# Kernel tuning notes

Hardware: AMD Instinct MI355X
Metric: run time of the kernel (lower is better)

The kernel has to match this reference:

```python
import jax, jax.numpy as jnp
import numpy as np

HIDDEN = 4096
NH = 32          # num query heads
NKV = 8          # num kv heads
HD = HIDDEN // NH  # 128
THETA = 10000.0
L = 4096         # llama_context_len (attention-sink window)
BS = 16          # paged KV block size
B = 16           # decode batch
MAXB = 385       # blocks per sequence
NBLOCKS = B * MAXB
CTX = 6145       # context_len for every sequence (num_past = 6144)


def rope(x, pos):
    """Neox-style RoPE. x: [..., H, HD]; pos: broadcastable to x.shape[:-2]."""
    half = HD // 2
    inv_freq = 1.0 / (THETA ** (jnp.arange(half, dtype=jnp.float32) * 2.0 / HD))
    ang = pos.astype(jnp.float32)[..., None] * inv_freq      # [..., half]
    cos = jnp.cos(ang)[..., None, :]                          # [..., 1, half]
    sin = jnp.sin(ang)[..., None, :]
    x1, x2 = x[..., :half], x[..., half:]
    return jnp.concatenate([x1 * cos - x2 * sin, x2 * cos + x1 * sin], axis=-1)


def setup_inputs() -> dict:
    key = jax.random.key(0)
    ks = jax.random.split(key, 6)
    hidden_states = jax.random.normal(ks[0], (B, HIDDEN), jnp.float32)
    positions = jax.random.randint(ks[1], (B,), 0, CTX).astype(jnp.int32)
    key_cache = jax.random.normal(ks[2], (NBLOCKS, NKV, HD, BS), jnp.float32)
    value_cache = jax.random.normal(ks[3], (NBLOCKS, NKV, HD, BS), jnp.float32)
    block_tables = jnp.arange(B * MAXB, dtype=jnp.int32).reshape(B, MAXB)
    w_qkv = jax.random.normal(ks[4], (HIDDEN, (NH + 2 * NKV) * HD), jnp.float32) * 0.02
    w_o = jax.random.normal(ks[5], (NH * HD, HIDDEN), jnp.float32) * 0.02
    return {
        "positions": positions,
        "hidden_states": hidden_states,
        "key_cache": key_cache,
        "value_cache": value_cache,
        "block_tables": block_tables,
        "context_len": CTX,
        "w_qkv": w_qkv,
        "w_o": w_o,
    }


def reference(positions, hidden_states, key_cache, value_cache, block_tables,
              context_len, w_qkv, w_o):
    # ---- qkv projection + split ----
    qkv = hidden_states @ w_qkv
    q, k, v = jnp.split(qkv, [NH * HD, NH * HD + NKV * HD], axis=-1)
    # ---- clamp positions to sink window and rope current q, k ----
    clamped = jnp.minimum(positions, L - 1)
    q = rope(q.reshape(B, NH, HD), clamped)          # [B, NH, HD]
    k = rope(k.reshape(B, NKV, HD), clamped)         # [B, NKV, HD]
    v = v.reshape(B, NKV, HD)

    # ---- static sink-window geometry (context_len is a Python int) ----
    num_past = context_len - 1
    blocks_to_ignore = (num_past - L) // BS + 1
    start = num_past - L + 1 + BS
    end = num_past

    # capped block table: token t<BS -> sink block bt[0];
    # t>=BS -> bt[blocks_to_ignore + t//BS]
    t = jnp.arange(L)
    logical = jnp.where(t < BS, 0, blocks_to_ignore + t // BS)   # [L]
    offset = t % BS                                              # [L]
    abs_pos = logical * BS + offset                              # [L] absolute position in seq

    phys = block_tables[:, logical]                              # [B, L]
    K = key_cache[phys, :, :, offset]                            # [B, L, NKV, HD]
    V = value_cache[phys, :, :, offset]

    # ---- sink RoPE rewrite: keys in [start, end) get an extra rotation at abs_pos-start ----
    rot_mask = (abs_pos >= start) & (abs_pos < end)
    K = jnp.where(rot_mask[None, :, None, None], rope(K, abs_pos - start), K)

    # ---- current token's freshly-rotated k/v occupy slot abs_pos == num_past ----
    cur = (abs_pos == num_past)
    K = jnp.where(cur[None, :, None, None], k[:, None, :, :], K)
    V = jnp.where(cur[None, :, None, None], v[:, None, :, :], V)

    # ---- GQA paged-decode attention over the 4096-token capped window ----
    valid = abs_pos <= num_past                                  # [L]
    G = NH // NKV
    qg = q.reshape(B, NKV, G, HD)
    scores = jnp.einsum('bkgd,blkd->bkgl', qg, K) * (HD ** -0.5)
    scores = jnp.where(valid[None, None, None, :], scores, jnp.finfo(scores.dtype).min)
    p = jax.nn.softmax(scores, axis=-1)
    attn = jnp.einsum('bkgl,blkd->bkgd', p, V).reshape(B, NH * HD)
    return attn @ w_o


if __name__ == "__main__":
    out = reference(**setup_inputs())
    print(out.shape, out.dtype)
```

## Files before the change

### kernel.cpp

```cpp
#include <hip/hip_runtime.h>
#include <math.h>

#define B_      16
#define NH      32
#define NKV     8
#define HD      128
#define GQ      4
#define LWIN    4096
#define BS      16
#define MAXB    385
#define HIDDEN  4096
#define QKV_COLS 6144
#define TAB_N   4100
#define T_CUR   4080
#define KS      64
#define NSPLIT  64
#define NCHUNK  8
#define SCALE   0.088388347648318447f
#define LOG1E4  9.210340371976184
#define TWO_PI  6.283185307179586
#define INV_2PI 0.15915494309189535

typedef float f4v __attribute__((ext_vector_type(4)));

__global__ __launch_bounds__(128, 1) void k_gemm_qkv(
    const float* __restrict__ X, const float* __restrict__ W,
    float* __restrict__ part,
    float* __restrict__ ctab, float* __restrict__ stab,
    float* __restrict__ pk, float* __restrict__ pv) {
  int tid = threadIdx.x;
  int k0 = blockIdx.y * KS;
  int n4 = (blockIdx.x * 128 + tid) * 4;
  f4v acc[B_];
#pragma unroll
  for (int b = 0; b < B_; b++) acc[b] = (f4v){0.f, 0.f, 0.f, 0.f};
  const float* wp = W + (size_t)k0 * QKV_COLS + n4;
  const float* xp = X + k0;
#pragma unroll
  for (int batch = 0; batch < KS / 16; batch++) {
    f4v w[16];
#pragma unroll
    for (int i = 0; i < 16; i++)
      w[i] = *(const f4v*)&wp[(size_t)(batch * 16 + i) * QKV_COLS];
#pragma unroll
    for (int i = 0; i < 16; i++) {
      int kk = batch * 16 + i;
#pragma unroll
      for (int b = 0; b < B_; b++) {
        float x = xp[b * HIDDEN + kk];
        acc[b][0] = fmaf(x, w[i][0], acc[b][0]);
        acc[b][1] = fmaf(x, w[i][1], acc[b][1]);
        acc[b][2] = fmaf(x, w[i][2], acc[b][2]);
        acc[b][3] = fmaf(x, w[i][3], acc[b][3]);
      }
    }
  }
  float* pp = part + (size_t)blockIdx.y * B_ * QKV_COLS + n4;
#pragma unroll
  for (int b = 0; b < B_; b++) *(f4v*)&pp[(size_t)b * QKV_COLS] = acc[b];

  int idx = (blockIdx.y * gridDim.x + blockIdx.x) * 128 + tid;
  if (idx < 64 * (TAB_N / 4)) {
    int d = idx / (TAB_N / 4);
    int q = idx - d * (TAB_N / 4);
    int i0 = q * 4;
    double f = exp(-(double)d / 64.0 * LOG1E4);
    double a = (double)(i0 - 1) * f;
    double rev = a * INV_2PI;
    rev -= rint(rev);
    float r = (float)(rev * TWO_PI);
    float c = cosf(r), s = sinf(r);
    float ff = (float)f;
    float cf = cosf(ff), sf = sinf(ff);
    int base = d * TAB_N + i0;
    ctab[base] = c; stab[base] = s;
#pragma unroll
    for (int j = 1; j < 4; j++) {
      float cn = c * cf - s * sf;
      float sn = s * cf + c * sf;
      c = cn; s = sn;
      ctab[base + j] = c; stab[base + j] = s;
    }
  }
  for (int z = idx; z < B_ * NKV * HD * BS; z += 98304) { pk[z] = 0.f; pv[z] = 0.f; }
}

__global__ __launch_bounds__(256) void k_qkv_finish(
    const float* __restrict__ part, const int* __restrict__ positions,
    const float* __restrict__ ctab, const float* __restrict__ stab,
    float* __restrict__ qout, float* __restrict__ pk, float* __restrict__ pv) {
  int idx = blockIdx.x * 256 + threadIdx.x;
  int b = idx / 3584;
  int u = idx - b * 3584;
  if (b >= B_) return;
  if (u < 2560) {
    int h = u >> 6, j = u & 63;
    int c1 = h * 128 + j;
    int c2 = c1 + 64;
    float s1 = 0.f, s2 = 0.f;
#pragma unroll 8
    for (int ky = 0; ky < NSPLIT; ky++) {
      const float* p = part + ((size_t)ky * B_ + b) * QKV_COLS;
      s1 += p[c1];
      s2 += p[c2];
    }
    int pos = min(positions[b], LWIN - 1);
    float c = ctab[j * TAB_N + pos + 1];
    float s = stab[j * TAB_N + pos + 1];
    float o1 = s1 * c - s2 * s;
    float o2 = s2 * c + s1 * s;
    if (h < NH) {
      qout[b * HIDDEN + c1] = o1;
      qout[b * HIDDEN + c2] = o2;
    } else {
      int kv = h - NH;
      pk[((b * NKV + kv) * HD + j) * BS] = o1;
      pk[((b * NKV + kv) * HD + j + 64) * BS] = o2;
    }
  } else {
    int vi = u - 2560;
    int kv = vi >> 7, d = vi & 127;
    int col = 5120 + vi;
    float s = 0.f;
#pragma unroll 8
    for (int ky = 0; ky < NSPLIT; ky++)
      s += part[((size_t)ky * B_ + b) * QKV_COLS + col];
    pv[((b * NKV + kv) * HD + d) * BS] = s;
  }
}

__global__ __launch_bounds__(128, 1) void k_attn(
    const float* __restrict__ kc, const float* __restrict__ vc,
    const int* __restrict__ bt, const float* __restrict__ qbuf,
    const float* __restrict__ pk, const float* __restrict__ pv,
    const float* __restrict__ ctab, const float* __restrict__ stab,
    float* __restrict__ partial) {
  __shared__ __align__(16) float qT[HD][GQ];
  __shared__ __align__(16) float p_s[512][GQ];
  __shared__ float redm[2][GQ];
  __shared__ float redl[2][GQ];
  __shared__ const float* kbase[32];
  __shared__ const float* vbase[32];

  int bx = blockIdx.x;
  int b = bx & 15, kv = bx >> 4;
  int chunk = blockIdx.y;
  int tid = threadIdx.x;
  int lane = tid & 63, wave = tid >> 6;

  for (int i = tid; i < GQ * HD; i += 128) {
    int g = i >> 7, d = i & 127;
    qT[d][g] = qbuf[b * HIDDEN + (kv * GQ + g) * HD + d];
  }
  if (tid < 32) {
    int tb = chunk * 32 + tid;
    if (tb == 255) {
      kbase[tid] = pk + (size_t)(b * NKV + kv) * (HD * BS);
      vbase[tid] = pv + (size_t)(b * NKV + kv) * (HD * BS);
    } else {
      int lg = (tb == 0) ? 0 : (129 + tb);
      size_t off = ((size_t)bt[b * MAXB + lg] * NKV + kv) * (HD * BS);
      kbase[tid] = kc + off;
      vbase[tid] = vc + off;
    }
  }
  __syncthreads();

  int blk_i = lane & 15, qq = lane >> 4;
  int t0 = chunk * 512 + wave * 256 + blk_i * 16 + qq * 4;
  const float* kb = kbase[wave * 16 + blk_i] + qq * 4;
  bool rot = (t0 >= 16) && (t0 < T_CUR);
  const float* ctp = ctab + t0;
  const float* stp = stab + t0;

  float sc[GQ][4];
#pragma unroll
  for (int g = 0; g < GQ; g++)
#pragma unroll
    for (int c = 0; c < 4; c++) sc[g][c] = 0.f;

#pragma unroll
  for (int batch = 0; batch < 8; batch++) {
    f4v k1[8], k2[8], cv[8], sv[8];
#pragma unroll
    for (int i = 0; i < 8; i++) {
      int d = batch * 8 + i;
      k1[i] = *(const f4v*)(kb + d * BS);
      k2[i] = *(const f4v*)(kb + (d + 64) * BS);
      cv[i] = *(const f4v*)(ctp + d * TAB_N);
      sv[i] = *(const f4v*)(stp + d * TAB_N);
    }
#pragma unroll
    for (int i = 0; i < 8; i++) {
      int d = batch * 8 + i;
      float4 q1 = *(const float4*)&qT[d][0];
      float4 q2 = *(const float4*)&qT[d + 64][0];
      float qg1[4] = {q1.x, q1.y, q1.z, q1.w};
      float qg2[4] = {q2.x, q2.y, q2.z, q2.w};
#pragma unroll
      for (int c = 0; c < 4; c++) {
        float cc = rot ? cv[i][c] : 1.f;
        float ss = rot ? sv[i][c] : 0.f;
        float r1 = k1[i][c] * cc - k2[i][c] * ss;
        float r2 = k2[i][c] * cc + k1[i][c] * ss;
#pragma unroll
        for (int g = 0; g < GQ; g++)
          sc[g][c] = fmaf(qg1[g], r1, fmaf(qg2[g], r2, sc[g][c]));
      }
    }
  }

  float mloc[GQ];
#pragma unroll
  for (int g = 0; g < GQ; g++) {
    float m = -3e38f;
#pragma unroll
    for (int c = 0; c < 4; c++) {
      float s = (t0 + c <= T_CUR) ? sc[g][c] * SCALE : -3e38f;
      sc[g][c] = s;
      m = fmaxf(m, s);
    }
#pragma unroll
    for (int off = 1; off < 64; off <<= 1) m = fmaxf(m, __shfl_xor(m, off, 64));
    mloc[g] = m;
  }
  if (lane == 0) {
#pragma unroll
    for (int g = 0; g < GQ; g++) redm[wave][g] = mloc[g];
  }
  __syncthreads();
  float mb[GQ];
#pragma unroll
  for (int g = 0; g < GQ; g++) mb[g] = fmaxf(redm[0][g], redm[1][g]);

  float4 prc[4];
  float ls[GQ] = {0.f, 0.f, 0.f, 0.f};
#pragma unroll
  for (int c = 0; c < 4; c++) {
    float p0 = __expf(sc[0][c] - mb[0]);
    float p1 = __expf(sc[1][c] - mb[1]);
    float p2 = __expf(sc[2][c] - mb[2]);
    float p3 = __expf(sc[3][c] - mb[3]);
    ls[0] += p0; ls[1] += p1; ls[2] += p2; ls[3] += p3;
    prc[c] = make_float4(p0, p1, p2, p3);
  }
#pragma unroll
  for (int g = 0; g < GQ; g++) {
    float v = ls[g];
#pragma unroll
    for (int off = 1; off < 64; off <<= 1) v += __shfl_xor(v, off, 64);
    ls[g] = v;
  }
  if (lane == 0) {
#pragma unroll
    for (int g = 0; g < GQ; g++) redl[wave][g] = ls[g];
  }
  int trow = t0 - chunk * 512;
#pragma unroll
  for (int c = 0; c < 4; c++) *(float4*)&p_s[trow + c][0] = prc[c];
  __syncthreads();

  float acc0 = 0.f, acc1 = 0.f, acc2 = 0.f, acc3 = 0.f;
  int d_own = tid;
#pragma unroll
  for (int bt4 = 0; bt4 < 8; bt4++) {
    f4v vr[4][4];
#pragma unroll
    for (int t = 0; t < 4; t++) {
      const float* vb = vbase[bt4 * 4 + t] + d_own * BS;
      vr[t][0] = *(const f4v*)(vb);
      vr[t][1] = *(const f4v*)(vb + 4);
      vr[t][2] = *(const f4v*)(vb + 8);
      vr[t][3] = *(const f4v*)(vb + 12);
    }
#pragma unroll
    for (int t = 0; t < 4; t++) {
      const float* pp = &p_s[(bt4 * 4 + t) * 16][0];
#pragma unroll
      for (int jq = 0; jq < 4; jq++) {
#pragma unroll
        for (int j = 0; j < 4; j++) {
          float4 pj = *(const float4*)(pp + (jq * 4 + j) * GQ);
          float vv = vr[t][jq][j];
          acc0 = fmaf(pj.x, vv, acc0);
          acc1 = fmaf(pj.y, vv, acc1);
          acc2 = fmaf(pj.z, vv, acc2);
          acc3 = fmaf(pj.w, vv, acc3);
        }
      }
    }
  }

  int pid = b * NKV + kv;
  float* pw = partial + ((size_t)pid * NCHUNK + chunk) * (GQ * 130);
  pw[0 * 130 + 2 + d_own] = acc0;
  pw[1 * 130 + 2 + d_own] = acc1;
  pw[2 * 130 + 2 + d_own] = acc2;
  pw[3 * 130 + 2 + d_own] = acc3;
  if (tid == 0) {
#pragma unroll
    for (int g = 0; g < GQ; g++) {
      pw[g * 130 + 0] = mb[g];
      pw[g * 130 + 1] = redl[0][g] + redl[1][g];
    }
  }
}

__global__ __launch_bounds__(128, 1) void k_gemm_o(
    const float* __restrict__ apart, const float* __restrict__ W,
    float* __restrict__ part) {
  __shared__ __align__(16) float xs[B_][KS];
  __shared__ float wexp[B_][NCHUNK];
  __shared__ float lw[B_];

  int tid = threadIdx.x;
  int k0 = blockIdx.y * KS;
  int h = k0 >> 7, kv = h >> 2, g = h & 3, d0 = k0 & 127;

  if (tid < B_) {
    int b = tid;
    const float* pb = apart + ((size_t)(b * NKV + kv) * NCHUNK) * (GQ * 130) + g * 130;
    float M = -3e38f;
#pragma unroll
    for (int c = 0; c < NCHUNK; c++) M = fmaxf(M, pb[c * (GQ * 130)]);
    float L = 0.f;
#pragma unroll
    for (int c = 0; c < NCHUNK; c++) {
      float w = __expf(pb[c * (GQ * 130)] - M);
      wexp[b][c] = w;
      L = fmaf(pb[c * (GQ * 130) + 1], w, L);
    }
    lw[b] = L;
  }
  __syncthreads();

#pragma unroll
  for (int it = 0; it < 8; it++) {
    int item = it * 128 + tid;
    int b = item >> 6, kk = item & 63;
    const float* pb = apart + ((size_t)(b * NKV + kv) * NCHUNK) * (GQ * 130) + g * 130 + 2 + d0 + kk;
    float val = 0.f;
#pragma unroll
    for (int c = 0; c < NCHUNK; c++) val = fmaf(pb[c * (GQ * 130)], wexp[b][c], val);
    xs[b][kk] = val / lw[b];
  }
  __syncthreads();

  int n4 = (blockIdx.x * 128 + tid) * 4;
  f4v acc[B_];
#pragma unroll
  for (int b = 0; b < B_; b++) acc[b] = (f4v){0.f, 0.f, 0.f, 0.f};
  const float* wp = W + (size_t)k0 * HIDDEN + n4;
#pragma unroll
  for (int batch = 0; batch < KS / 16; batch++) {
    f4v w[16];
#pragma unroll
    for (int i = 0; i < 16; i++)
      w[i] = *(const f4v*)&wp[(size_t)(batch * 16 + i) * HIDDEN];
#pragma unroll
    for (int i = 0; i < 16; i++) {
      int kk = batch * 16 + i;
#pragma unroll
      for (int b = 0; b < B_; b++) {
        float x = xs[b][kk];
        acc[b][0] = fmaf(x, w[i][0], acc[b][0]);
        acc[b][1] = fmaf(x, w[i][1], acc[b][1]);
        acc[b][2] = fmaf(x, w[i][2], acc[b][2]);
        acc[b][3] = fmaf(x, w[i][3], acc[b][3]);
      }
    }
  }
  float* pp = part + (size_t)blockIdx.y * B_ * HIDDEN + n4;
#pragma unroll
  for (int b = 0; b < B_; b++) *(f4v*)&pp[(size_t)b * HIDDEN] = acc[b];
}

__global__ __launch_bounds__(256) void k_reduce_out(
    const float* __restrict__ part, float* __restrict__ out) {
  int idx = blockIdx.x * 256 + threadIdx.x;
  int b = idx >> 12, n = idx & 4095;
  float s = 0.f;
#pragma unroll 8
  for (int ky = 0; ky < NSPLIT; ky++)
    s += part[((size_t)ky * B_ + b) * HIDDEN + n];
  out[idx] = s;
}

extern "C" void kernel_launch(void* const* d_in, const int* in_sizes, int n_in,
                              void* d_out, int out_size, void* d_ws, size_t ws_size,
                              hipStream_t stream) {
  const int*   positions = (const int*)d_in[0];
  const float* hs        = (const float*)d_in[1];
  const float* kc        = (const float*)d_in[2];
  const float* vc        = (const float*)d_in[3];
  const int*   bt        = (const int*)d_in[4];
  const float* w_qkv     = (const float*)d_in[6];
  const float* w_o       = (const float*)d_in[7];
  float* out = (float*)d_out;

  float* ws    = (float*)d_ws;
  float* ctab  = ws;
  float* stab  = ctab + 262400;
  float* pk    = stab + 262400;
  float* pv    = pk + 262144;
  float* qbuf  = pv + 262144;
  float* apart = qbuf + 65536;
  float* gpart = apart + 532480;

  k_gemm_qkv<<<dim3(QKV_COLS / 512, NSPLIT), 128, 0, stream>>>(
      hs, w_qkv, gpart, ctab, stab, pk, pv);
  k_qkv_finish<<<(B_ * 3584) / 256, 256, 0, stream>>>(gpart, positions, ctab, stab, qbuf, pk, pv);
  k_attn<<<dim3(B_ * NKV, NCHUNK), 128, 0, stream>>>(kc, vc, bt, qbuf, pk, pv, ctab, stab, apart);
  k_gemm_o<<<dim3(HIDDEN / 512, NSPLIT), 128, 0, stream>>>(apart, w_o, gpart);
  k_reduce_out<<<(B_ * HIDDEN) / 256, 256, 0, stream>>>(gpart, out);
}
```

Before: 208.5 us.

## Stage K blocks through double-buffered LDS and split head-dim across threads

The QK score phase now copies two 16-token K blocks per iteration into a double-buffered shared-memory tile with coalesced loads, prefetching the next pair into registers while computing the current one. Each thread handles one token and a quarter of the head dimension, and partial dot products are combined by shuffle and shared memory before being written to p_s. This is meant to replace strided per-thread global K loads with coalesced staging and overlap loads with compute. In exchange it adds two barriers per iteration (32 in total), scalar rather than vector cos/sin table reads, and an extra shared-memory reduction step.

```diff
diff --git a/kernel.cpp b/kernel.cpp
--- a/kernel.cpp
+++ b/kernel.cpp
@@ -16,6 +16,7 @@
 #define KS      64
 #define NSPLIT  64
 #define NCHUNK  8
+#define KSTR    2064
 #define SCALE   0.088388347648318447f
 #define LOG1E4  9.210340371976184
 #define TWO_PI  6.283185307179586
@@ -135,8 +136,10 @@
     const float* __restrict__ pk, const float* __restrict__ pv,
     const float* __restrict__ ctab, const float* __restrict__ stab,
     float* __restrict__ partial) {
+  __shared__ __align__(16) float kst[2][2][KSTR];
   __shared__ __align__(16) float qT[HD][GQ];
   __shared__ __align__(16) float p_s[512][GQ];
+  __shared__ __align__(16) float sps[32][GQ];
   __shared__ float redm[2][GQ];
   __shared__ float redl[2][GQ];
   __shared__ const float* kbase[32];
@@ -166,50 +169,86 @@
   }
   __syncthreads();
 
-  int blk_i = lane & 15, qq = lane >> 4;
-  int t0 = chunk * 512 + wave * 256 + blk_i * 16 + qq * 4;
-  const float* kb = kbase[wave * 16 + blk_i] + qq * 4;
-  bool rot = (t0 >= 16) && (t0 < T_CUR);
-  const float* ctp = ctab + t0;
-  const float* stp = stab + t0;
-
-  float sc[GQ][4];
-#pragma unroll
-  for (int g = 0; g < GQ; g++)
-#pragma unroll
-    for (int c = 0; c < 4; c++) sc[g][c] = 0.f;
-
-#pragma unroll
-  for (int batch = 0; batch < 8; batch++) {
-    f4v k1[8], k2[8], cv[8], sv[8];
-#pragma unroll
-    for (int i = 0; i < 8; i++) {
-      int d = batch * 8 + i;
-      k1[i] = *(const f4v*)(kb + d * BS);
-      k2[i] = *(const f4v*)(kb + (d + 64) * BS);
-      cv[i] = *(const f4v*)(ctp + d * TAB_N);
-      sv[i] = *(const f4v*)(stp + d * TAB_N);
-    }
-#pragma unroll
-    for (int i = 0; i < 8; i++) {
-      int d = batch * 8 + i;
+  int t32 = tid & 31;
+  int dq  = tid >> 5;
+  f4v st0[4], st1[4];
+
+  {
+    const float* kb0 = kbase[0];
+    const float* kb1 = kbase[1];
+#pragma unroll
+    for (int i = 0; i < 4; i++) st0[i] = *(const f4v*)(kb0 + tid * 16 + i * 4);
+#pragma unroll
+    for (int i = 0; i < 4; i++) st1[i] = *(const f4v*)(kb1 + tid * 16 + i * 4);
+#pragma unroll
+    for (int i = 0; i < 4; i++) *(f4v*)&kst[0][0][tid * 16 + i * 4] = st0[i];
+#pragma unroll
+    for (int i = 0; i < 4; i++) *(f4v*)&kst[0][1][tid * 16 + i * 4] = st1[i];
+  }
+  __syncthreads();
+
+  for (int it = 0; it < 16; it++) {
+    int cur = it & 1;
+    if (it < 15) {
+      const float* kb0 = kbase[(it + 1) * 2];
+      const float* kb1 = kbase[(it + 1) * 2 + 1];
+#pragma unroll
+      for (int i = 0; i < 4; i++) st0[i] = *(const f4v*)(kb0 + tid * 16 + i * 4);
+#pragma unroll
+      for (int i = 0; i < 4; i++) st1[i] = *(const f4v*)(kb1 + tid * 16 + i * 4);
+    }
+    int tg = chunk * 512 + it * 32 + t32;
+    bool rot = (tg >= 16) && (tg < T_CUR);
+    int blk = t32 >> 4, tt = t32 & 15;
+    const float* kcl = &kst[cur][blk][0];
+    float sc0 = 0.f, sc1 = 0.f, sc2 = 0.f, sc3 = 0.f;
+#pragma unroll
+    for (int i = 0; i < 16; i++) {
+      int d = dq * 16 + i;
+      float k1 = kcl[d * 16 + tt];
+      float k2 = kcl[(d + 64) * 16 + tt];
+      float cc = rot ? ctab[d * TAB_N + tg] : 1.f;
+      float ss = rot ? stab[d * TAB_N + tg] : 0.f;
+      float r1 = k1 * cc - k2 * ss;
+      float r2 = k2 * cc + k1 * ss;
       float4 q1 = *(const float4*)&qT[d][0];
       float4 q2 = *(const float4*)&qT[d + 64][0];
-      float qg1[4] = {q1.x, q1.y, q1.z, q1.w};
-      float qg2[4] = {q2.x, q2.y, q2.z, q2.w};
-#pragma unroll
-      for (int c = 0; c < 4; c++) {
-        float cc = rot ? cv[i][c] : 1.f;
-        float ss = rot ? sv[i][c] : 0.f;
-        float r1 = k1[i][c] * cc - k2[i][c] * ss;
-        float r2 = k2[i][c] * cc + k1[i][c] * ss;
-#pragma unroll
-        for (int g = 0; g < GQ; g++)
-          sc[g][c] = fmaf(qg1[g], r1, fmaf(qg2[g], r2, sc[g][c]));
-      }
-    }
-  }
-
+      sc0 = fmaf(q1.x, r1, fmaf(q2.x, r2, sc0));
+      sc1 = fmaf(q1.y, r1, fmaf(q2.y, r2, sc1));
+      sc2 = fmaf(q1.z, r1, fmaf(q2.z, r2, sc2));
+      sc3 = fmaf(q1.w, r1, fmaf(q2.w, r2, sc3));
+    }
+    sc0 += __shfl_xor(sc0, 32, 64);
+    sc1 += __shfl_xor(sc1, 32, 64);
+    sc2 += __shfl_xor(sc2, 32, 64);
+    sc3 += __shfl_xor(sc3, 32, 64);
+    if (wave == 1 && lane < 32)
+      *(float4*)&sps[lane][0] = make_float4(sc0, sc1, sc2, sc3);
+    __syncthreads();
+    if (wave == 0 && lane < 32) {
+      float4 o = *(const float4*)&sps[lane][0];
+      *(float4*)&p_s[it * 32 + lane][0] =
+          make_float4(sc0 + o.x, sc1 + o.y, sc2 + o.z, sc3 + o.w);
+    }
+    if (it < 15) {
+      int nxt = cur ^ 1;
+#pragma unroll
+      for (int i = 0; i < 4; i++) *(f4v*)&kst[nxt][0][tid * 16 + i * 4] = st0[i];
+#pragma unroll
+      for (int i = 0; i < 4; i++) *(f4v*)&kst[nxt][1][tid * 16 + i * 4] = st1[i];
+    }
+    __syncthreads();
+  }
+
+  int blk_i = lane & 15, qq = lane >> 4;
+  int trow = wave * 256 + blk_i * 16 + qq * 4;
+  int t0 = chunk * 512 + trow;
+  float sc[GQ][4];
+#pragma unroll
+  for (int c = 0; c < 4; c++) {
+    float4 r = *(const float4*)&p_s[trow + c][0];
+    sc[0][c] = r.x; sc[1][c] = r.y; sc[2][c] = r.z; sc[3][c] = r.w;
+  }
   float mloc[GQ];
 #pragma unroll
   for (int g = 0; g < GQ; g++) {
@@ -255,7 +294,6 @@
 #pragma unroll
     for (int g = 0; g < GQ; g++) redl[wave][g] = ls[g];
   }
-  int trow = t0 - chunk * 512;
 #pragma unroll
   for (int c = 0; c < 4; c++) *(float4*)&p_s[trow + c][0] = prc[c];
   __syncthreads();
```

New measurement: 214.4 us. +2.8%, slower.
